# Kernel optimization log

Measured on AMD Instinct MI355X. Metric: run time of the kernel, lower is better.

## Reference

```python
import jax, jax.numpy as jnp
import numpy as np

B, S, HID = 2, 2048, 2048
NH, NKV = 32, 8
HD = HID // NH          # 64
G = NH // NKV           # 4 query heads per kv head
ROPE_BASE = 10000.0


def _rope_cos_sin(seq_len, head_dim, dtype):
    inv_freq = 1.0 / (ROPE_BASE ** (jnp.arange(0, head_dim, 2, dtype=jnp.float32) / head_dim))
    freqs = jnp.arange(seq_len, dtype=jnp.float32)[:, None] * inv_freq[None, :]  # [S, HD/2]
    cos = jnp.cos(freqs)
    sin = jnp.sin(freqs)
    # torch code does cos.repeat(1, 2): tile along last dim -> [S, HD]
    cos = jnp.concatenate([cos, cos], axis=-1).astype(dtype)
    sin = jnp.concatenate([sin, sin], axis=-1).astype(dtype)
    return cos, sin


def _rotate_half(x):
    x1, x2 = jnp.split(x, 2, axis=-1)
    return jnp.concatenate([-x2, x1], axis=-1)


def setup_inputs() -> dict:
    key = jax.random.key(0)
    ks = jax.random.split(key, 5)
    sc = 0.02
    return {
        "hidden_states": jax.random.normal(ks[0], (B, S, HID), dtype=jnp.float32),
        "wq": jax.random.normal(ks[1], (HID, HID), dtype=jnp.float32) * sc,
        "wk": jax.random.normal(ks[2], (NKV * HD, HID), dtype=jnp.float32) * sc,
        "wv": jax.random.normal(ks[3], (NKV * HD, HID), dtype=jnp.float32) * sc,
        "wo": jax.random.normal(ks[4], (HID, HID), dtype=jnp.float32) * sc,
    }


def reference(hidden_states, wq, wk, wv, wo):
    b, s, _ = hidden_states.shape
    # projections (torch Linear: y = x @ W^T)
    q = (hidden_states @ wq.T).reshape(b, s, NH, HD).transpose(0, 2, 1, 3)   # [B,NH,S,HD]
    k = (hidden_states @ wk.T).reshape(b, s, NKV, HD).transpose(0, 2, 1, 3)  # [B,NKV,S,HD]
    v = (hidden_states @ wv.T).reshape(b, s, NKV, HD).transpose(0, 2, 1, 3)  # [B,NKV,S,HD]

    cos, sin = _rope_cos_sin(s, HD, q.dtype)  # [S,HD]
    q = q * cos + _rotate_half(q) * sin
    k = k * cos + _rotate_half(k) * sin

    # GQA: group query heads per kv head instead of repeat_interleave (same math)
    qg = q.reshape(b, NKV, G, s, HD)
    scale = HD ** -0.5
    scores = jnp.einsum('bkgsd,bktd->bkgst', qg, k) * scale     # [B,NKV,G,S,S]
    attn = jax.nn.softmax(scores, axis=-1)
    out = jnp.einsum('bkgst,bktd->bkgsd', attn, v)              # [B,NKV,G,S,HD]
    out = out.reshape(b, NH, s, HD).transpose(0, 2, 1, 3).reshape(b, s, HID)
    return out @ wo.T
```

## Files before the change

### kernel.cpp

```cpp
#include <hip/hip_runtime.h>
#include <stdint.h>

typedef __attribute__((ext_vector_type(8))) short bf16x8;
typedef __attribute__((ext_vector_type(4))) short bf16x4;
typedef __attribute__((ext_vector_type(4))) float f32x4;
typedef __attribute__((ext_vector_type(4))) unsigned u32x4;
typedef __attribute__((ext_vector_type(2))) unsigned u32x2;

#define S_LEN 2048
#define HIDDEN 2048
#define N_HEADS 32
#define N_KV 8
#define HEAD_DIM 64
#define KVD (N_KV * HEAD_DIM)

__device__ __forceinline__ float bf2f(short u) {
  return __builtin_bit_cast(float, ((unsigned)(unsigned short)u) << 16);
}
__device__ __forceinline__ short f2bf(float f) {
  unsigned u = __builtin_bit_cast(unsigned, f);
  u += 0x7FFFu + ((u >> 16) & 1u);
  return (short)(u >> 16);
}
__device__ __forceinline__ unsigned cvtpk(float lo, float hi) {
  unsigned r;
  asm("v_cvt_pk_bf16_f32 %0, %1, %2" : "=v"(r) : "v"(lo), "v"(hi));
  return r;
}
__device__ __forceinline__ bf16x8 cvt8(f32x4 lo, f32x4 hi) {
  bf16x8 r;
#pragma unroll
  for (int j = 0; j < 4; ++j) { r[j] = f2bf(lo[j]); r[j + 4] = f2bf(hi[j]); }
  return r;
}
__device__ __forceinline__ void storeC(float* p, float v) { *p = v; }
__device__ __forceinline__ void storeC(short* p, float v) { *p = f2bf(v); }

__device__ __forceinline__ void gll16(const void* g, void* l) {
  __builtin_amdgcn_global_load_lds(
      (const __attribute__((address_space(1))) void*)g,
      (__attribute__((address_space(3))) void*)l, 16, 0, 0);
}

struct CvtArgs {
  const float* src[5];
  short* dst[5];
  int cnt4[5];
};
__global__ void cvt_bf16(CvtArgs a, int total4) {
  int u = blockIdx.x * 256 + threadIdx.x;
  const int stride = gridDim.x * 256;
  for (; u < total4; u += stride) {
    int s = 0, off = u;
    while (off >= a.cnt4[s]) { off -= a.cnt4[s]; ++s; }
    f32x4 v = *(const f32x4*)(a.src[s] + (size_t)off * 4);
    bf16x4 r;
#pragma unroll
    for (int j = 0; j < 4; ++j) r[j] = f2bf(v[j]);
    *(bf16x4*)(a.dst[s] + (size_t)off * 4) = r;
  }
}

template <typename CT>
__launch_bounds__(256, 3)
__global__ void gemm_lds(const short* __restrict__ A, const short* __restrict__ W,
                         CT* __restrict__ C, int M, int N, int K) {
  __shared__ short As[128 * 32];
  __shared__ short Ws[128 * 32];
  const int tid  = threadIdx.x;
  const int lane = tid & 63;
  const int w    = tid >> 6;
  const int wm = w >> 1, wn = w & 1;
  const int lr = lane & 15, lg = lane >> 4;

  int bx = blockIdx.x, by = blockIdx.y;
  {
    const int nwg = gridDim.x * gridDim.y;
    if ((nwg & 7) == 0) {
      const int bid = by * gridDim.x + bx;
      const int id2 = (bid & 7) * (nwg >> 3) + (bid >> 3);
      bx = id2 % gridDim.x;
      by = id2 / gridDim.x;
    }
  }
  const int m0 = by * 128, n0 = bx * 128;

  const size_t a0 = (size_t)(m0 + w * 16 + (lane >> 2)) * K + (lane & 3) * 8;
  const size_t a1 = a0 + (size_t)64 * K;
  const size_t b0 = (size_t)(n0 + w * 16 + (lane >> 2)) * K + (lane & 3) * 8;
  const size_t b1 = b0 + (size_t)64 * K;
  short* lA0 = &As[(w * 16) * 32];
  short* lA1 = &As[(64 + w * 16) * 32];
  short* lB0 = &Ws[(w * 16) * 32];
  short* lB1 = &Ws[(64 + w * 16) * 32];

  f32x4 acc[4][4] = {};

  for (int k0 = 0; k0 < K; k0 += 32) {
    __syncthreads();
    gll16(A + a0 + k0, lA0);
    gll16(A + a1 + k0, lA1);
    gll16(W + b0 + k0, lB0);
    gll16(W + b1 + k0, lB1);
    __syncthreads();
    bf16x8 af[4], bfr[4];
#pragma unroll
    for (int i = 0; i < 4; ++i) {
      af[i]  = *(const bf16x8*)&As[(wm * 64 + i * 16 + lr) * 32 + lg * 8];
      bfr[i] = *(const bf16x8*)&Ws[(wn * 64 + i * 16 + lr) * 32 + lg * 8];
    }
#pragma unroll
    for (int i = 0; i < 4; ++i)
#pragma unroll
      for (int j = 0; j < 4; ++j)
        acc[i][j] = __builtin_amdgcn_mfma_f32_16x16x32_bf16(af[i], bfr[j], acc[i][j], 0, 0, 0);
  }

#pragma unroll
  for (int i = 0; i < 4; ++i)
#pragma unroll
    for (int j = 0; j < 4; ++j) {
      const int row = m0 + wm * 64 + i * 16 + lg * 4;
      const int col = n0 + wn * 64 + j * 16 + lr;
#pragma unroll
      for (int r = 0; r < 4; ++r)
        storeC(&C[(size_t)(row + r) * N + col], acc[i][j][r]);
    }
}

template <typename AT, typename CT>
__launch_bounds__(256, 2)
__global__ void gemm_bt(const AT* __restrict__ A, const float* __restrict__ W,
                        CT* __restrict__ C, int M, int N, int K) {
  __shared__ short As[128][40];
  __shared__ short Ws[128][40];
  const int tid  = threadIdx.x;
  const int lane = tid & 63;
  const int wid  = tid >> 6;
  const int wm = wid >> 1, wn = wid & 1;
  const int lr = lane & 15, lg = lane >> 4;
  const int m0 = blockIdx.y * 128, n0 = blockIdx.x * 128;
  const int srow = tid >> 2;
  const int scol = (tid & 3) * 8;

  f32x4 acc[4][4] = {};
  const AT*    Ap = A + (size_t)(m0 + srow) * K + scol;
  const float* Wp = W + (size_t)(n0 + srow) * K + scol;

  for (int k0 = 0; k0 < K; k0 += 32) {
    bf16x8 a0, a1, b0, b1;
    if constexpr (sizeof(AT) == 4) {
      a0 = cvt8(*(const f32x4*)(Ap + k0), *(const f32x4*)(Ap + k0 + 4));
      a1 = cvt8(*(const f32x4*)(Ap + (size_t)64 * K + k0),
                *(const f32x4*)(Ap + (size_t)64 * K + k0 + 4));
    } else {
      a0 = *(const bf16x8*)(Ap + k0);
      a1 = *(const bf16x8*)(Ap + (size_t)64 * K + k0);
    }
    b0 = cvt8(*(const f32x4*)(Wp + k0), *(const f32x4*)(Wp + k0 + 4));
    b1 = cvt8(*(const f32x4*)(Wp + (size_t)64 * K + k0),
              *(const f32x4*)(Wp + (size_t)64 * K + k0 + 4));
    __syncthreads();
    *(bf16x8*)&As[srow][scol]      = a0;
    *(bf16x8*)&As[srow + 64][scol] = a1;
    *(bf16x8*)&Ws[srow][scol]      = b0;
    *(bf16x8*)&Ws[srow + 64][scol] = b1;
    __syncthreads();
    bf16x8 af[4], bfr[4];
#pragma unroll
    for (int i = 0; i < 4; ++i) {
      af[i]  = *(const bf16x8*)&As[wm * 64 + i * 16 + lr][lg * 8];
      bfr[i] = *(const bf16x8*)&Ws[wn * 64 + i * 16 + lr][lg * 8];
    }
#pragma unroll
    for (int i = 0; i < 4; ++i)
#pragma unroll
      for (int j = 0; j < 4; ++j)
        acc[i][j] = __builtin_amdgcn_mfma_f32_16x16x32_bf16(af[i], bfr[j], acc[i][j], 0, 0, 0);
  }
#pragma unroll
  for (int i = 0; i < 4; ++i)
#pragma unroll
    for (int j = 0; j < 4; ++j) {
      const int row = m0 + wm * 64 + i * 16 + lg * 4;
      const int col = n0 + wn * 64 + j * 16 + lr;
#pragma unroll
      for (int r = 0; r < 4; ++r)
        storeC(&C[(size_t)(row + r) * N + col], acc[i][j][r]);
    }
}

template <int NH>
__global__ void rope_kernel(short* __restrict__ buf, int rowstride, int total) {
  int idx = blockIdx.x * 256 + threadIdx.x;
  if (idx >= total) return;
  const int i   = idx & 31;
  const int hh  = (idx >> 5) % NH;
  const int row = (idx >> 5) / NH;
  const int pos = row & (S_LEN - 1);
  const float invf = exp2f(-(float)i * (13.287712379549449f / 32.0f));
  const float ang  = (float)pos * invf;
  float sn, c;
  sincosf(ang, &sn, &c);
  size_t base = (size_t)row * rowstride + hh * 64;
  float x1 = bf2f(buf[base + i]);
  float x2 = bf2f(buf[base + i + 32]);
  buf[base + i]      = f2bf(x1 * c - x2 * sn);
  buf[base + i + 32] = f2bf(x2 * c + x1 * sn);
}

__device__ __forceinline__ void qkt_mfma(const bf16x8 (&kf)[4][2],
                                         const bf16x8 (&qa)[2][2],
                                         f32x4 (&sf)[2][4]) {
  __builtin_amdgcn_s_setprio(1);
#pragma unroll
  for (int nf = 0; nf < 4; ++nf)
#pragma unroll
    for (int fr = 0; fr < 2; ++fr) {
      f32x4 t = {};
      t = __builtin_amdgcn_mfma_f32_16x16x32_bf16(kf[nf][0], qa[fr][0], t, 0, 0, 0);
      t = __builtin_amdgcn_mfma_f32_16x16x32_bf16(kf[nf][1], qa[fr][1], t, 0, 0, 0);
      sf[fr][nf] = t;
    }
  __builtin_amdgcn_s_setprio(0);
}

__device__ __forceinline__ void load_kf(bf16x8 (&kf)[4][2], const short* kbase,
                                        int t, int ks_) {
  const short* kp = kbase + (size_t)t * 64 * ks_;
#pragma unroll
  for (int nf = 0; nf < 4; ++nf) {
    kf[nf][0] = *(const bf16x8*)(kp + (size_t)nf * 16 * ks_);
    kf[nf][1] = *(const bf16x8*)(kp + (size_t)nf * 16 * ks_ + 32);
  }
}

__device__ __forceinline__ void softmax_pv(
    f32x4 (&sf)[2][4], const short (*vt)[72], f32x4 (&o)[2][4],
    float (&mrow)[2], float (&msc)[2], float (&lsum)[2],
    int lr, int lg, float SC, float THRR) {
  bf16x8 pa[2][2];
#pragma unroll
  for (int fr = 0; fr < 2; ++fr) {
    float lmax = fmaxf(fmaxf(sf[fr][0][0], sf[fr][0][1]), fmaxf(sf[fr][0][2], sf[fr][0][3]));
#pragma unroll
    for (int nf = 1; nf < 4; ++nf) {
      float m01 = fmaxf(sf[fr][nf][0], sf[fr][nf][1]);
      float m23 = fmaxf(sf[fr][nf][2], sf[fr][nf][3]);
      lmax = fmaxf(lmax, fmaxf(m01, m23));
    }
    if (!__all(lmax <= mrow[fr] + THRR)) {
      float mx = fmaxf(lmax, __shfl_xor(lmax, 16));
      mx = fmaxf(mx, __shfl_xor(mx, 32));
      const float mnew  = fmaxf(mrow[fr], mx);
      const float alpha = exp2f((mrow[fr] - mnew) * SC);
      mrow[fr] = mnew;
      msc[fr]  = mnew * SC;
      lsum[fr] *= alpha;
#pragma unroll
      for (int df = 0; df < 4; ++df) o[fr][df] *= alpha;
    }
    const float nm = msc[fr];
    float s = 0.f;
#pragma unroll
    for (int nf = 0; nf < 4; ++nf)
#pragma unroll
      for (int r = 0; r < 4; ++r) {
        float pv = exp2f(fmaf(sf[fr][nf][r], SC, -nm));
        sf[fr][nf][r] = pv;
        s += pv;
      }
    lsum[fr] += s;
#pragma unroll
    for (int ks2 = 0; ks2 < 2; ++ks2) {
      u32x4 pk;
      pk[0] = cvtpk(sf[fr][2 * ks2][0], sf[fr][2 * ks2][1]);
      pk[1] = cvtpk(sf[fr][2 * ks2][2], sf[fr][2 * ks2][3]);
      pk[2] = cvtpk(sf[fr][2 * ks2 + 1][0], sf[fr][2 * ks2 + 1][1]);
      pk[3] = cvtpk(sf[fr][2 * ks2 + 1][2], sf[fr][2 * ks2 + 1][3]);
      pa[fr][ks2] = __builtin_bit_cast(bf16x8, pk);
    }
  }
  __builtin_amdgcn_s_setprio(1);
#pragma unroll
  for (int ks2 = 0; ks2 < 2; ++ks2) {
    bf16x8 vb[4];
#pragma unroll
    for (int df = 0; df < 4; ++df)
      vb[df] = *(const bf16x8*)&vt[df * 16 + lr][ks2 * 32 + lg * 8];
#pragma unroll
    for (int fr = 0; fr < 2; ++fr)
#pragma unroll
      for (int df = 0; df < 4; ++df)
        o[fr][df] = __builtin_amdgcn_mfma_f32_16x16x32_bf16(vb[df], pa[fr][ks2], o[fr][df], 0, 0, 0);
  }
  __builtin_amdgcn_s_setprio(0);
}

#define NT (S_LEN / 64)
__launch_bounds__(256, 2)
__global__ void attn_kernel(const short* __restrict__ Q, const short* __restrict__ K,
                            const short* __restrict__ V, short* __restrict__ O,
                            int qs, int ks_, int os) {
  const int qt = blockIdx.x, h = blockIdx.y, b = blockIdx.z;
  const int kv = h >> 2;
  const int tid  = threadIdx.x;
  const int lane = tid & 63, w = tid >> 6;
  const int lr = lane & 15, lg = lane >> 4;

  __shared__ short Vt[2][64][72];

  const int q0 = qt * 128 + w * 32;
  bf16x8 qa[2][2];
#pragma unroll
  for (int fr = 0; fr < 2; ++fr) {
    const short* qp = Q + (size_t)(b * S_LEN + q0 + fr * 16 + lr) * qs + h * HEAD_DIM + lg * 8;
    qa[fr][0] = *(const bf16x8*)qp;
    qa[fr][1] = *(const bf16x8*)(qp + 32);
  }

  f32x4 o[2][4] = {};
  float mrow[2] = {-1e30f, -1e30f};
  float msc[2]  = {-1e30f, -1e30f};
  float lsum[2] = {0.f, 0.f};

  const int vdb   = w * 16;
  const int cperm = (lane & 32) + ((lane >> 2) & 3) * 8 + ((lane >> 4) & 1) * 4 + (lane & 3);
  const short* vbase = V + ((size_t)(b * S_LEN) + lane) * ks_ + kv * HEAD_DIM + vdb;
  const short* kbase = K + (size_t)(b * S_LEN + lr) * ks_ + kv * HEAD_DIM + lg * 8;

  const float SC   = 0.125f * 1.4426950408889634f;
  const float THRR = 8.0f / SC;

  bf16x8 vp0 = *(const bf16x8*)vbase;
  bf16x8 vp1 = *(const bf16x8*)(vbase + 8);
  bf16x8 kf[4][2];
  f32x4 sfA[2][4], sfB[2][4];
  load_kf(kf, kbase, 0, ks_);
  qkt_mfma(kf, qa, sfA);
  load_kf(kf, kbase, 1, ks_);

  for (int t = 0; t < NT; t += 2) {
#pragma unroll
    for (int j = 0; j < 8; ++j) Vt[0][vdb + j][cperm] = vp0[j];
#pragma unroll
    for (int j = 0; j < 8; ++j) Vt[0][vdb + 8 + j][cperm] = vp1[j];
    __syncthreads();
    {
      const short* vp = vbase + (size_t)(t + 1) * 64 * ks_;
      vp0 = *(const bf16x8*)vp;
      vp1 = *(const bf16x8*)(vp + 8);
    }
    qkt_mfma(kf, qa, sfB);
    if (t + 2 < NT) load_kf(kf, kbase, t + 2, ks_);
    softmax_pv(sfA, Vt[0], o, mrow, msc, lsum, lr, lg, SC, THRR);

#pragma unroll
    for (int j = 0; j < 8; ++j) Vt[1][vdb + j][cperm] = vp0[j];
#pragma unroll
    for (int j = 0; j < 8; ++j) Vt[1][vdb + 8 + j][cperm] = vp1[j];
    __syncthreads();
    if (t + 2 < NT) {
      const short* vp = vbase + (size_t)(t + 2) * 64 * ks_;
      vp0 = *(const bf16x8*)vp;
      vp1 = *(const bf16x8*)(vp + 8);
      qkt_mfma(kf, qa, sfA);
    }
    if (t + 3 < NT) load_kf(kf, kbase, t + 3, ks_);
    softmax_pv(sfB, Vt[1], o, mrow, msc, lsum, lr, lg, SC, THRR);
  }

#pragma unroll
  for (int fr = 0; fr < 2; ++fr) {
    float ls = lsum[fr];
    ls += __shfl_xor(ls, 16);
    ls += __shfl_xor(ls, 32);
    const float invl = 1.0f / ls;
    const size_t orow = (size_t)(b * S_LEN + q0 + fr * 16 + lr) * os + h * HEAD_DIM;
#pragma unroll
    for (int df = 0; df < 4; ++df) {
      u32x2 pk;
      pk[0] = cvtpk(o[fr][df][0] * invl, o[fr][df][1] * invl);
      pk[1] = cvtpk(o[fr][df][2] * invl, o[fr][df][3] * invl);
      *(u32x2*)&O[orow + df * 16 + 4 * lg] = pk;
    }
  }
}

extern "C" void kernel_launch(void* const* d_in, const int* in_sizes, int n_in,
                              void* d_out, int out_size, void* d_ws, size_t ws_size,
                              hipStream_t stream) {
  (void)in_sizes; (void)n_in; (void)out_size;
  const float* hidden = (const float*)d_in[0];
  const float* wq = (const float*)d_in[1];
  const float* wk = (const float*)d_in[2];
  const float* wv = (const float*)d_in[3];
  const float* wo = (const float*)d_in[4];
  float* out = (float*)d_out;

  const int M = 2 * S_LEN;
  const size_t nHid  = (size_t)M * HIDDEN;
  const size_t nW    = (size_t)HIDDEN * HIDDEN;
  const size_t nWkv  = (size_t)KVD * HIDDEN;
  const size_t nWcat = nW + 2 * nWkv;
  const int    NQKV  = HIDDEN + 2 * KVD;
  const size_t nQKV  = (size_t)M * NQKV;

  const size_t fastElems = nHid + nWcat + nW + nQKV + nHid;
  if (ws_size >= fastElems * sizeof(short)) {
    short* hb   = (short*)d_ws;
    short* wcat = hb + nHid;
    short* wob  = wcat + nWcat;
    short* QKV  = wob + nW;
    short* AO   = QKV + nQKV;

    CvtArgs ca;
    ca.src[0] = hidden; ca.dst[0] = hb;            ca.cnt4[0] = (int)(nHid / 4);
    ca.src[1] = wq;     ca.dst[1] = wcat;          ca.cnt4[1] = (int)(nW / 4);
    ca.src[2] = wk;     ca.dst[2] = wcat + nW;     ca.cnt4[2] = (int)(nWkv / 4);
    ca.src[3] = wv;     ca.dst[3] = wcat + nW + nWkv; ca.cnt4[3] = (int)(nWkv / 4);
    ca.src[4] = wo;     ca.dst[4] = wob;           ca.cnt4[4] = (int)(nW / 4);
    const int total4 = (int)((nHid + nWcat + nW) / 4);
    cvt_bf16<<<2048, 256, 0, stream>>>(ca, total4);

    gemm_lds<short><<<dim3(NQKV / 128, 32), 256, 0, stream>>>(hb, wcat, QKV, M, NQKV, HIDDEN);
    const int rtot = M * 40 * 32;
    rope_kernel<40><<<(rtot + 255) / 256, 256, 0, stream>>>(QKV, NQKV, rtot);
    attn_kernel<<<dim3(S_LEN / 128, N_HEADS, 2), 256, 0, stream>>>(
        QKV, QKV + HIDDEN, QKV + HIDDEN + KVD, AO, NQKV, NQKV, HIDDEN);
    gemm_lds<float><<<dim3(16, 32), 256, 0, stream>>>(AO, wob, out, M, HIDDEN, HIDDEN);
  } else {
    short* Qb = (short*)d_ws;
    short* Kb = Qb + nHid;
    short* Vb = Kb + (size_t)M * KVD;
    short* AO = Vb + (size_t)M * KVD;
    gemm_bt<float, short><<<dim3(16, 32), 256, 0, stream>>>(hidden, wq, Qb, M, HIDDEN, HIDDEN);
    gemm_bt<float, short><<<dim3(4, 32), 256, 0, stream>>>(hidden, wk, Kb, M, KVD, HIDDEN);
    gemm_bt<float, short><<<dim3(4, 32), 256, 0, stream>>>(hidden, wv, Vb, M, KVD, HIDDEN);
    const int rq = M * N_HEADS * 32, rk = M * N_KV * 32;
    rope_kernel<N_HEADS><<<(rq + 255) / 256, 256, 0, stream>>>(Qb, HIDDEN, rq);
    rope_kernel<N_KV><<<(rk + 255) / 256, 256, 0, stream>>>(Kb, KVD, rk);
    attn_kernel<<<dim3(S_LEN / 128, N_HEADS, 2), 256, 0, stream>>>(
        Qb, Kb, Vb, AO, HIDDEN, KVD, HIDDEN);
    gemm_bt<short, float><<<dim3(16, 32), 256, 0, stream>>>(AO, wo, out, M, HIDDEN, HIDDEN);
  }
}
```

Measured before the change: 293.0 us.

## Hoist V LDS reads before softmax, template strides, drop GEMM tile swizzle

The attention kernel now reads V fragments from LDS right after each barrier into registers, so the LDS latency can overlap the QK^T MFMAs and softmax instead of stalling the PV MFMAs. Row strides become template constants so address arithmetic folds at compile time. The GEMM block-index remapping for L2 locality is removed in favour of plain blockIdx mapping. The extra V fragment registers raise register pressure and may reduce occupancy, and dropping the swizzle could hurt cache reuse in the GEMMs.

```diff
diff --git a/kernel.cpp b/kernel.cpp
--- a/kernel.cpp
+++ b/kernel.cpp
@@ -72,18 +72,7 @@
   const int w    = tid >> 6;
   const int wm = w >> 1, wn = w & 1;
   const int lr = lane & 15, lg = lane >> 4;
-
-  int bx = blockIdx.x, by = blockIdx.y;
-  {
-    const int nwg = gridDim.x * gridDim.y;
-    if ((nwg & 7) == 0) {
-      const int bid = by * gridDim.x + bx;
-      const int id2 = (bid & 7) * (nwg >> 3) + (bid >> 3);
-      bx = id2 % gridDim.x;
-      by = id2 / gridDim.x;
-    }
-  }
-  const int m0 = by * 128, n0 = bx * 128;
+  const int m0 = blockIdx.y * 128, n0 = blockIdx.x * 128;
 
   const size_t a0 = (size_t)(m0 + w * 16 + (lane >> 2)) * K + (lane & 3) * 8;
   const size_t a1 = a0 + (size_t)64 * K;
@@ -225,20 +214,29 @@
   __builtin_amdgcn_s_setprio(0);
 }
 
-__device__ __forceinline__ void load_kf(bf16x8 (&kf)[4][2], const short* kbase,
-                                        int t, int ks_) {
-  const short* kp = kbase + (size_t)t * 64 * ks_;
+template <int KS>
+__device__ __forceinline__ void load_kf(bf16x8 (&kf)[4][2], const short* kbase, int t) {
+  const short* kp = kbase + (size_t)t * 64 * KS;
 #pragma unroll
   for (int nf = 0; nf < 4; ++nf) {
-    kf[nf][0] = *(const bf16x8*)(kp + (size_t)nf * 16 * ks_);
-    kf[nf][1] = *(const bf16x8*)(kp + (size_t)nf * 16 * ks_ + 32);
-  }
+    kf[nf][0] = *(const bf16x8*)(kp + (size_t)nf * 16 * KS);
+    kf[nf][1] = *(const bf16x8*)(kp + (size_t)nf * 16 * KS + 32);
+  }
+}
+
+__device__ __forceinline__ void load_vb(bf16x8 (&vb)[2][4], const short (*vt)[72],
+                                        int lr, int lg) {
+#pragma unroll
+  for (int ks2 = 0; ks2 < 2; ++ks2)
+#pragma unroll
+    for (int df = 0; df < 4; ++df)
+      vb[ks2][df] = *(const bf16x8*)&vt[df * 16 + lr][ks2 * 32 + lg * 8];
 }
 
 __device__ __forceinline__ void softmax_pv(
-    f32x4 (&sf)[2][4], const short (*vt)[72], f32x4 (&o)[2][4],
+    f32x4 (&sf)[2][4], const bf16x8 (&vb)[2][4], f32x4 (&o)[2][4],
     float (&mrow)[2], float (&msc)[2], float (&lsum)[2],
-    int lr, int lg, float SC, float THRR) {
+    float SC, float THRR) {
   bf16x8 pa[2][2];
 #pragma unroll
   for (int fr = 0; fr < 2; ++fr) {
@@ -283,25 +281,20 @@
   }
   __builtin_amdgcn_s_setprio(1);
 #pragma unroll
-  for (int ks2 = 0; ks2 < 2; ++ks2) {
-    bf16x8 vb[4];
-#pragma unroll
-    for (int df = 0; df < 4; ++df)
-      vb[df] = *(const bf16x8*)&vt[df * 16 + lr][ks2 * 32 + lg * 8];
+  for (int ks2 = 0; ks2 < 2; ++ks2)
 #pragma unroll
     for (int fr = 0; fr < 2; ++fr)
 #pragma unroll
       for (int df = 0; df < 4; ++df)
-        o[fr][df] = __builtin_amdgcn_mfma_f32_16x16x32_bf16(vb[df], pa[fr][ks2], o[fr][df], 0, 0, 0);
-  }
+        o[fr][df] = __builtin_amdgcn_mfma_f32_16x16x32_bf16(vb[ks2][df], pa[fr][ks2], o[fr][df], 0, 0, 0);
   __builtin_amdgcn_s_setprio(0);
 }
 
 #define NT (S_LEN / 64)
+template <int QS, int KS, int OS>
 __launch_bounds__(256, 2)
 __global__ void attn_kernel(const short* __restrict__ Q, const short* __restrict__ K,
-                            const short* __restrict__ V, short* __restrict__ O,
-                            int qs, int ks_, int os) {
+                            const short* __restrict__ V, short* __restrict__ O) {
   const int qt = blockIdx.x, h = blockIdx.y, b = blockIdx.z;
   const int kv = h >> 2;
   const int tid  = threadIdx.x;
@@ -314,7 +307,7 @@
   bf16x8 qa[2][2];
 #pragma unroll
   for (int fr = 0; fr < 2; ++fr) {
-    const short* qp = Q + (size_t)(b * S_LEN + q0 + fr * 16 + lr) * qs + h * HEAD_DIM + lg * 8;
+    const short* qp = Q + (size_t)(b * S_LEN + q0 + fr * 16 + lr) * QS + h * HEAD_DIM + lg * 8;
     qa[fr][0] = *(const bf16x8*)qp;
     qa[fr][1] = *(const bf16x8*)(qp + 32);
   }
@@ -326,8 +319,8 @@
 
   const int vdb   = w * 16;
   const int cperm = (lane & 32) + ((lane >> 2) & 3) * 8 + ((lane >> 4) & 1) * 4 + (lane & 3);
-  const short* vbase = V + ((size_t)(b * S_LEN) + lane) * ks_ + kv * HEAD_DIM + vdb;
-  const short* kbase = K + (size_t)(b * S_LEN + lr) * ks_ + kv * HEAD_DIM + lg * 8;
+  const short* vbase = V + ((size_t)(b * S_LEN) + lane) * KS + kv * HEAD_DIM + vdb;
+  const short* kbase = K + (size_t)(b * S_LEN + lr) * KS + kv * HEAD_DIM + lg * 8;
 
   const float SC   = 0.125f * 1.4426950408889634f;
   const float THRR = 8.0f / SC;
@@ -335,10 +328,11 @@
   bf16x8 vp0 = *(const bf16x8*)vbase;
   bf16x8 vp1 = *(const bf16x8*)(vbase + 8);
   bf16x8 kf[4][2];
+  bf16x8 vbA[2][4], vbB[2][4];
   f32x4 sfA[2][4], sfB[2][4];
-  load_kf(kf, kbase, 0, ks_);
+  load_kf<KS>(kf, kbase, 0);
   qkt_mfma(kf, qa, sfA);
-  load_kf(kf, kbase, 1, ks_);
+  load_kf<KS>(kf, kbase, 1);
 
   for (int t = 0; t < NT; t += 2) {
 #pragma unroll
@@ -346,28 +340,30 @@
 #pragma unroll
     for (int j = 0; j < 8; ++j) Vt[0][vdb + 8 + j][cperm] = vp1[j];
     __syncthreads();
+    load_vb(vbA, Vt[0], lr, lg);
     {
-      const short* vp = vbase + (size_t)(t + 1) * 64 * ks_;
+      const short* vp = vbase + (size_t)(t + 1) * 64 * KS;
       vp0 = *(const bf16x8*)vp;
       vp1 = *(const bf16x8*)(vp + 8);
     }
     qkt_mfma(kf, qa, sfB);
-    if (t + 2 < NT) load_kf(kf, kbase, t + 2, ks_);
-    softmax_pv(sfA, Vt[0], o, mrow, msc, lsum, lr, lg, SC, THRR);
+    if (t + 2 < NT) load_kf<KS>(kf, kbase, t + 2);
+    softmax_pv(sfA, vbA, o, mrow, msc, lsum, SC, THRR);
 
 #pragma unroll
     for (int j = 0; j < 8; ++j) Vt[1][vdb + j][cperm] = vp0[j];
 #pragma unroll
     for (int j = 0; j < 8; ++j) Vt[1][vdb + 8 + j][cperm] = vp1[j];
     __syncthreads();
+    load_vb(vbB, Vt[1], lr, lg);
     if (t + 2 < NT) {
-      const short* vp = vbase + (size_t)(t + 2) * 64 * ks_;
+      const short* vp = vbase + (size_t)(t + 2) * 64 * KS;
       vp0 = *(const bf16x8*)vp;
       vp1 = *(const bf16x8*)(vp + 8);
       qkt_mfma(kf, qa, sfA);
     }
-    if (t + 3 < NT) load_kf(kf, kbase, t + 3, ks_);
-    softmax_pv(sfB, Vt[1], o, mrow, msc, lsum, lr, lg, SC, THRR);
+    if (t + 3 < NT) load_kf<KS>(kf, kbase, t + 3);
+    softmax_pv(sfB, vbB, o, mrow, msc, lsum, SC, THRR);
   }
 
 #pragma unroll
@@ -376,7 +372,7 @@
     ls += __shfl_xor(ls, 16);
     ls += __shfl_xor(ls, 32);
     const float invl = 1.0f / ls;
-    const size_t orow = (size_t)(b * S_LEN + q0 + fr * 16 + lr) * os + h * HEAD_DIM;
+    const size_t orow = (size_t)(b * S_LEN + q0 + fr * 16 + lr) * OS + h * HEAD_DIM;
 #pragma unroll
     for (int df = 0; df < 4; ++df) {
       u32x2 pk;
@@ -426,8 +422,8 @@
     gemm_lds<short><<<dim3(NQKV / 128, 32), 256, 0, stream>>>(hb, wcat, QKV, M, NQKV, HIDDEN);
     const int rtot = M * 40 * 32;
     rope_kernel<40><<<(rtot + 255) / 256, 256, 0, stream>>>(QKV, NQKV, rtot);
-    attn_kernel<<<dim3(S_LEN / 128, N_HEADS, 2), 256, 0, stream>>>(
-        QKV, QKV + HIDDEN, QKV + HIDDEN + KVD, AO, NQKV, NQKV, HIDDEN);
+    attn_kernel<3072, 3072, HIDDEN><<<dim3(S_LEN / 128, N_HEADS, 2), 256, 0, stream>>>(
+        QKV, QKV + HIDDEN, QKV + HIDDEN + KVD, AO);
     gemm_lds<float><<<dim3(16, 32), 256, 0, stream>>>(AO, wob, out, M, HIDDEN, HIDDEN);
   } else {
     short* Qb = (short*)d_ws;
@@ -440,8 +436,8 @@
     const int rq = M * N_HEADS * 32, rk = M * N_KV * 32;
     rope_kernel<N_HEADS><<<(rq + 255) / 256, 256, 0, stream>>>(Qb, HIDDEN, rq);
     rope_kernel<N_KV><<<(rk + 255) / 256, 256, 0, stream>>>(Kb, KVD, rk);
-    attn_kernel<<<dim3(S_LEN / 128, N_HEADS, 2), 256, 0, stream>>>(
-        Qb, Kb, Vb, AO, HIDDEN, KVD, HIDDEN);
+    attn_kernel<HIDDEN, KVD, HIDDEN><<<dim3(S_LEN / 128, N_HEADS, 2), 256, 0, stream>>>(
+        Qb, Kb, Vb, AO);
     gemm_bt<short, float><<<dim3(16, 32), 256, 0, stream>>>(AO, wo, out, M, HIDDEN, HIDDEN);
   }
 }
```

Result: no change. 289.1 us (-1.3%).
